# Performance work log

Hardware: AMD Instinct MI355X
Metric: run time of the kernel (lower is better)

## Reference

```python
import jax, jax.numpy as jnp
import numpy as np

HEADS = 16
HEAD_DIM = 64
DIM = 1024
INNER = HEADS * HEAD_DIM  # 1024


def rotate_half(t):
    # split last dim into two halves, return cat(-x2, x1)
    x1, x2 = jnp.split(t, 2, axis=-1)
    return jnp.concatenate((-x2, x1), axis=-1)


def rope_table(n, head_dim, dtype):
    inv_freq = 1.0 / (10000.0 ** (jnp.arange(0, head_dim, 2, dtype=jnp.float32) / head_dim))
    freqs = jnp.arange(n, dtype=jnp.float32)[:, None] * inv_freq[None, :]  # [n, hd/2]
    return jnp.concatenate((freqs, freqs), axis=-1).astype(dtype)  # [n, hd]


def setup_inputs() -> dict:
    key = jax.random.key(0)
    k1, k2, k3, k4 = jax.random.split(key, 4)
    x = jax.random.normal(k1, (1, 4096, DIM), dtype=jnp.float32)
    s = 0.02
    W_qkv = jax.random.normal(k2, (DIM, 3 * INNER), dtype=jnp.float32) * s
    W_o1 = jax.random.normal(k3, (INNER, DIM), dtype=jnp.float32) * s
    W_o2 = jax.random.normal(k4, (DIM, DIM), dtype=jnp.float32) * s
    gamma = jnp.ones((DIM,), dtype=jnp.float32)
    return {"x": x, "W_qkv": W_qkv, "W_o1": W_o1, "W_o2": W_o2, "gamma": gamma}


def reference(x, W_qkv, W_o1, W_o2, gamma):
    b, n, _ = x.shape
    scale = HEAD_DIM ** -0.5
    qkv = x @ W_qkv  # [b, n, 3*inner]
    q, k, v = jnp.split(qkv, 3, axis=-1)
    # [b, n, inner] -> [b, h, n, hd]
    to_heads = lambda t: t.reshape(b, n, HEADS, HEAD_DIM).transpose(0, 2, 1, 3)
    q, k, v = to_heads(q), to_heads(k), to_heads(v)

    pos = rope_table(n, HEAD_DIM, x.dtype)  # [n, hd]
    cos, sin = jnp.cos(pos), jnp.sin(pos)
    apply_rope = lambda t: t * cos + rotate_half(t) * sin
    q, k = apply_rope(q), apply_rope(k)

    dots = jnp.einsum('bhid,bhjd->bhij', q, k) * scale  # [b, h, n, n]
    causal = jnp.triu(jnp.ones((n, n), dtype=bool), 1)
    neg = -jnp.finfo(dots.dtype).max
    dots = jnp.where(causal, neg, dots)
    attn = jax.nn.softmax(dots, axis=-1)

    out = jnp.einsum('bhij,bhjd->bhid', attn, v)  # [b, h, n, hd]
    out = out.transpose(0, 2, 1, 3).reshape(b, n, INNER)
    # to_out: Linear -> ReLU -> Linear (dropout = identity in eval)
    out = jax.nn.relu(out @ W_o1) @ W_o2
    # AttnLayerNorm: layer_norm over last dim with gamma, beta=0
    mean = jnp.mean(out, axis=-1, keepdims=True)
    var = jnp.var(out, axis=-1, keepdims=True)
    out = (out - mean) * jax.lax.rsqrt(var + 1e-5) * gamma
    return out
```

## Files before the change

### kernel.cpp

```cpp
#include <hip/hip_runtime.h>
#include <hip/hip_bf16.h>
#include <float.h>
#include <math.h>

#define HEADS 16
#define HD 64
#define DIM 1024
#define NTOK 4096
#define QKVN 3072

typedef short s8v __attribute__((ext_vector_type(8)));
typedef float f4v __attribute__((ext_vector_type(4)));

static __device__ __forceinline__ unsigned short f2b(float f) {
  __hip_bfloat16 h = __float2bfloat16(f);
  unsigned short u;
  __builtin_memcpy(&u, &h, 2);
  return u;
}
static __device__ __forceinline__ s8v pack_bf8(float4 a, float4 b) {
  s8v r;
  r[0] = (short)f2b(a.x); r[1] = (short)f2b(a.y); r[2] = (short)f2b(a.z); r[3] = (short)f2b(a.w);
  r[4] = (short)f2b(b.x); r[5] = (short)f2b(b.y); r[6] = (short)f2b(b.z); r[7] = (short)f2b(b.w);
  return r;
}
static __device__ __forceinline__ void gload16(const unsigned short* g, unsigned short* l) {
  __builtin_amdgcn_global_load_lds(
      (const __attribute__((address_space(1))) void*)g,
      (__attribute__((address_space(3))) void*)l, 16, 0, 0);
}

__global__ __launch_bounds__(256) void cast_f2b(const float* __restrict__ in,
                                                unsigned short* __restrict__ out) {
  const int i = (blockIdx.x * 256 + threadIdx.x) * 8;
  float4 a = *(const float4*)(in + i);
  float4 b = *(const float4*)(in + i + 4);
  *(s8v*)(out + i) = pack_bf8(a, b);
}

__global__ __launch_bounds__(256) void transpose_f2b(const float* __restrict__ in,
                                                     unsigned short* __restrict__ out,
                                                     int K, int N) {
  __shared__ unsigned short T[32][36];
  const int k0 = blockIdx.y * 32, n0 = blockIdx.x * 32;
  const int t = threadIdx.x;
  const int r = t >> 3, c4 = (t & 7) * 4;
  float4 f = *(const float4*)(in + (size_t)(k0 + r) * N + n0 + c4);
  T[r][c4 + 0] = f2b(f.x);
  T[r][c4 + 1] = f2b(f.y);
  T[r][c4 + 2] = f2b(f.z);
  T[r][c4 + 3] = f2b(f.w);
  __syncthreads();
  ushort4 o;
  o.x = T[c4 + 0][r];
  o.y = T[c4 + 1][r];
  o.z = T[c4 + 2][r];
  o.w = T[c4 + 3][r];
  *(ushort4*)(out + (size_t)(n0 + r) * K + k0 + c4) = o;
}

template <int OUT_F32, int RELU>
__global__ __launch_bounds__(256) void gemm_bb(const unsigned short* __restrict__ A,
                                               const unsigned short* __restrict__ Bt,
                                               void* __restrict__ Cv,
                                               int M, int N, int K) {
  __shared__ __align__(16) unsigned short As[128 * 32];
  __shared__ __align__(16) unsigned short Bs[128 * 32];
  const int t = threadIdx.x;
  const int wave = t >> 6, lane = t & 63;
  const int wr = wave >> 1, wc = wave & 1;
  const int g = lane >> 4, c = lane & 15;
  const int m0 = blockIdx.y * 128, n0 = blockIdx.x * 128;

  const int sr = t >> 2;
  const int sc = (t & 3) * 8;

  const unsigned short* a0p = A + (size_t)(m0 + sr) * K + sc;
  const unsigned short* a1p = A + (size_t)(m0 + sr + 64) * K + sc;
  const unsigned short* b0p = Bt + (size_t)(n0 + sr) * K + sc;
  const unsigned short* b1p = Bt + (size_t)(n0 + sr + 64) * K + sc;
  unsigned short* lA0 = As + t * 8;
  unsigned short* lA1 = As + 2048 + t * 8;
  unsigned short* lB0 = Bs + t * 8;
  unsigned short* lB1 = Bs + 2048 + t * 8;

  f4v acc[4][4] = {};

  for (int k0 = 0; k0 < K; k0 += 32) {
    __syncthreads();
    gload16(a0p + k0, lA0);
    gload16(a1p + k0, lA1);
    gload16(b0p + k0, lB0);
    gload16(b1p + k0, lB1);
    __syncthreads();
    s8v af[4], bf[4];
#pragma unroll
    for (int m = 0; m < 4; ++m) af[m] = *(const s8v*)&As[(wr * 64 + m * 16 + c) * 32 + g * 8];
#pragma unroll
    for (int n = 0; n < 4; ++n) bf[n] = *(const s8v*)&Bs[(wc * 64 + n * 16 + c) * 32 + g * 8];
#pragma unroll
    for (int m = 0; m < 4; ++m)
#pragma unroll
      for (int n = 0; n < 4; ++n)
        acc[m][n] = __builtin_amdgcn_mfma_f32_16x16x32_bf16(af[m], bf[n], acc[m][n], 0, 0, 0);
  }

#pragma unroll
  for (int m = 0; m < 4; ++m)
#pragma unroll
    for (int n = 0; n < 4; ++n)
#pragma unroll
      for (int r = 0; r < 4; ++r) {
        const int row = m0 + wr * 64 + m * 16 + g * 4 + r;
        const int col = n0 + wc * 64 + n * 16 + c;
        float v = acc[m][n][r];
        if (RELU) v = fmaxf(v, 0.f);
        if (OUT_F32)
          ((float*)Cv)[(size_t)row * N + col] = v;
        else
          ((unsigned short*)Cv)[(size_t)row * N + col] = f2b(v);
      }
}

__global__ __launch_bounds__(512) void rope64_kernel(unsigned short* __restrict__ qkv) {
  __shared__ float cs[32], sn[32];
  const int i = blockIdx.x;
  const int t = threadIdx.x;
  if (t < 32) {
    const double inv = pow(10000.0, -(double)t / 32.0);
    double sd, cd;
    sincos((double)i * inv, &sd, &cd);
    cs[t] = (float)cd;
    sn[t] = (float)sd;
  }
  __syncthreads();
  const int h = t >> 5, j = t & 31;
  const float cc = cs[j], ss = sn[j];
  const size_t base = (size_t)i * QKVN + h * HD + j;
  const float qa = __bfloat162float(*(const __hip_bfloat16*)&qkv[base]);
  const float qb = __bfloat162float(*(const __hip_bfloat16*)&qkv[base + 32]);
  qkv[base] = f2b((qa * cc - qb * ss) * 0.125f);
  qkv[base + 32] = f2b((qb * cc + qa * ss) * 0.125f);
  const float ka = __bfloat162float(*(const __hip_bfloat16*)&qkv[base + DIM]);
  const float kb = __bfloat162float(*(const __hip_bfloat16*)&qkv[base + DIM + 32]);
  qkv[base + DIM] = f2b(ka * cc - kb * ss);
  qkv[base + DIM + 32] = f2b(kb * cc + ka * ss);
}

__global__ __launch_bounds__(256) void attn_mfma(const unsigned short* __restrict__ qkv,
                                                 unsigned short* __restrict__ att) {
  __shared__ unsigned short Ks[64][72];
  __shared__ unsigned short Vt[64][72];
  __shared__ unsigned short Pl[4][16][72];
  const int bid = blockIdx.x;
  const int h = bid & 15;
  const int qi = 63 - (bid >> 4);
  const int t = threadIdx.x;
  const int w = t >> 6, lane = t & 63;
  const int g = lane >> 4, c = lane & 15;
  const int q0 = qi * 64 + w * 16;

  s8v qf[2];
#pragma unroll
  for (int kf = 0; kf < 2; ++kf)
    qf[kf] = *(const s8v*)(qkv + (size_t)(q0 + c) * QKVN + h * HD + kf * 32 + g * 8);

  f4v O[4] = {};
  float mrow[4], lrow[4];
#pragma unroll
  for (int r = 0; r < 4; ++r) { mrow[r] = -1e30f; lrow[r] = 0.f; }

  const int ntile = qi + 1;
  for (int tile = 0; tile < ntile; ++tile) {
    const int kv0 = tile * 64;
    __syncthreads();
    {
      const int kr = t >> 3;
      const int kc = (t & 7) * 8;
#pragma unroll
      for (int it = 0; it < 2; ++it) {
        const int r = kr + it * 32;
        *(s8v*)&Ks[r][kc] =
            *(const s8v*)(qkv + (size_t)(kv0 + r) * QKVN + DIM + h * HD + kc);
      }
      const int kg = t & 15, dc = t >> 4;
      const unsigned short* vb = qkv + (size_t)(kv0 + 4 * kg) * QKVN + 2 * DIM + h * HD + dc * 4;
      ushort4 v0 = *(const ushort4*)(vb);
      ushort4 v1 = *(const ushort4*)(vb + QKVN);
      ushort4 v2 = *(const ushort4*)(vb + 2 * QKVN);
      ushort4 v3 = *(const ushort4*)(vb + 3 * QKVN);
      const unsigned short* r0 = (const unsigned short*)&v0;
      const unsigned short* r1 = (const unsigned short*)&v1;
      const unsigned short* r2 = (const unsigned short*)&v2;
      const unsigned short* r3 = (const unsigned short*)&v3;
#pragma unroll
      for (int dl = 0; dl < 4; ++dl) {
        ushort4 u;
        u.x = r0[dl]; u.y = r1[dl]; u.z = r2[dl]; u.w = r3[dl];
        *(ushort4*)&Vt[dc * 4 + dl][kg * 4] = u;
      }
    }
    __syncthreads();

    f4v S[4] = {};
#pragma unroll
    for (int n = 0; n < 4; ++n)
#pragma unroll
      for (int kf = 0; kf < 2; ++kf) {
        s8v kfr = *(const s8v*)&Ks[n * 16 + c][kf * 32 + g * 8];
        S[n] = __builtin_amdgcn_mfma_f32_16x16x32_bf16(qf[kf], kfr, S[n], 0, 0, 0);
      }

    float rmax[4] = {-1e30f, -1e30f, -1e30f, -1e30f};
    if (kv0 + 63 > q0) {
#pragma unroll
      for (int n = 0; n < 4; ++n)
#pragma unroll
        for (int r = 0; r < 4; ++r) {
          float s = S[n][r];
          const int col = kv0 + n * 16 + c;
          const int row = q0 + 4 * g + r;
          s = (col > row) ? -1e30f : s;
          S[n][r] = s;
          rmax[r] = fmaxf(rmax[r], s);
        }
    } else {
#pragma unroll
      for (int n = 0; n < 4; ++n)
#pragma unroll
        for (int r = 0; r < 4; ++r) rmax[r] = fmaxf(rmax[r], S[n][r]);
    }
#pragma unroll
    for (int r = 0; r < 4; ++r) {
      rmax[r] = fmaxf(rmax[r], __shfl_xor(rmax[r], 1));
      rmax[r] = fmaxf(rmax[r], __shfl_xor(rmax[r], 2));
      rmax[r] = fmaxf(rmax[r], __shfl_xor(rmax[r], 4));
      rmax[r] = fmaxf(rmax[r], __shfl_xor(rmax[r], 8));
    }

    bool upd = false;
#pragma unroll
    for (int r = 0; r < 4; ++r) upd = upd || (rmax[r] > mrow[r] + 8.0f);
    if (__any((int)upd)) {
#pragma unroll
      for (int r = 0; r < 4; ++r) {
        const float mn = fmaxf(mrow[r], rmax[r]);
        const float corr = __expf(mrow[r] - mn);
        mrow[r] = mn;
        lrow[r] *= corr;
#pragma unroll
        for (int n = 0; n < 4; ++n) O[n][r] *= corr;
      }
    }
    float rsum[4] = {0.f, 0.f, 0.f, 0.f};
#pragma unroll
    for (int n = 0; n < 4; ++n)
#pragma unroll
      for (int r = 0; r < 4; ++r) {
        const float p = __expf(S[n][r] - mrow[r]);
        rsum[r] += p;
        Pl[w][4 * g + r][n * 16 + c] = f2b(p);
      }
#pragma unroll
    for (int r = 0; r < 4; ++r) {
      rsum[r] += __shfl_xor(rsum[r], 1);
      rsum[r] += __shfl_xor(rsum[r], 2);
      rsum[r] += __shfl_xor(rsum[r], 4);
      rsum[r] += __shfl_xor(rsum[r], 8);
      lrow[r] += rsum[r];
    }

    s8v pf[2];
#pragma unroll
    for (int kf = 0; kf < 2; ++kf) pf[kf] = *(const s8v*)&Pl[w][c][kf * 32 + g * 8];
#pragma unroll
    for (int n = 0; n < 4; ++n)
#pragma unroll
      for (int kf = 0; kf < 2; ++kf) {
        s8v vf = *(const s8v*)&Vt[n * 16 + c][kf * 32 + g * 8];
        O[n] = __builtin_amdgcn_mfma_f32_16x16x32_bf16(pf[kf], vf, O[n], 0, 0, 0);
      }
  }

  float inv[4];
#pragma unroll
  for (int r = 0; r < 4; ++r) inv[r] = 1.f / lrow[r];
#pragma unroll
  for (int n = 0; n < 4; ++n)
#pragma unroll
    for (int r = 0; r < 4; ++r) {
      const int row = q0 + 4 * g + r;
      att[(size_t)row * DIM + h * HD + n * 16 + c] = f2b(O[n][r] * inv[r]);
    }
}

__global__ __launch_bounds__(256) void layernorm_kernel(const float* __restrict__ x,
                                                        const float* __restrict__ gamma,
                                                        float* __restrict__ out) {
  const int row = blockIdx.x;
  const int t = threadIdx.x;
  const float4 v = ((const float4*)(x + (size_t)row * DIM))[t];
  float s = v.x + v.y + v.z + v.w;
  float ss = v.x * v.x + v.y * v.y + v.z * v.z + v.w * v.w;
#pragma unroll
  for (int off = 32; off > 0; off >>= 1) {
    s += __shfl_xor(s, off);
    ss += __shfl_xor(ss, off);
  }
  __shared__ float red[8];
  const int wave = t >> 6, lane = t & 63;
  if (lane == 0) {
    red[wave] = s;
    red[4 + wave] = ss;
  }
  __syncthreads();
  const float S = red[0] + red[1] + red[2] + red[3];
  const float SS = red[4] + red[5] + red[6] + red[7];
  const float mean = S * (1.f / 1024.f);
  const float var = SS * (1.f / 1024.f) - mean * mean;
  const float r = rsqrtf(var + 1e-5f);
  const float4 g4 = ((const float4*)gamma)[t];
  float4 o;
  o.x = (v.x - mean) * r * g4.x;
  o.y = (v.y - mean) * r * g4.y;
  o.z = (v.z - mean) * r * g4.z;
  o.w = (v.w - mean) * r * g4.w;
  ((float4*)(out + (size_t)row * DIM))[t] = o;
}

extern "C" void kernel_launch(void* const* d_in, const int* in_sizes, int n_in,
                              void* d_out, int out_size, void* d_ws, size_t ws_size,
                              hipStream_t stream) {
  const float* x = (const float*)d_in[0];
  const float* Wqkv = (const float*)d_in[1];
  const float* Wo1 = (const float*)d_in[2];
  const float* Wo2 = (const float*)d_in[3];
  const float* gamma = (const float*)d_in[4];
  float* out = (float*)d_out;

  char* wsb = (char*)d_ws;
  unsigned short* xb = (unsigned short*)wsb;
  unsigned short* qkv = (unsigned short*)(wsb + 8388608ull);
  unsigned short* Wqkvt = (unsigned short*)(wsb + 33554432ull);
  unsigned short* Wo1t = (unsigned short*)(wsb + 39845888ull);
  unsigned short* Wo2t = (unsigned short*)(wsb + 41943040ull);
  unsigned short* att = (unsigned short*)wsb;
  unsigned short* h1 = (unsigned short*)(wsb + 8388608ull);
  float* h2 = (float*)(wsb + 16777216ull);

  cast_f2b<<<NTOK * DIM / (256 * 8), 256, 0, stream>>>(x, xb);
  transpose_f2b<<<dim3(QKVN / 32, DIM / 32), 256, 0, stream>>>(Wqkv, Wqkvt, DIM, QKVN);
  transpose_f2b<<<dim3(DIM / 32, DIM / 32), 256, 0, stream>>>(Wo1, Wo1t, DIM, DIM);
  transpose_f2b<<<dim3(DIM / 32, DIM / 32), 256, 0, stream>>>(Wo2, Wo2t, DIM, DIM);
  gemm_bb<0, 0><<<dim3(QKVN / 128, NTOK / 128), 256, 0, stream>>>(xb, Wqkvt, qkv, NTOK, QKVN, DIM);
  rope64_kernel<<<NTOK, 512, 0, stream>>>(qkv);
  attn_mfma<<<NTOK / 64 * HEADS, 256, 0, stream>>>(qkv, att);
  gemm_bb<0, 1><<<dim3(DIM / 128, NTOK / 128), 256, 0, stream>>>(att, Wo1t, h1, NTOK, DIM, DIM);
  gemm_bb<1, 0><<<dim3(DIM / 128, NTOK / 128), 256, 0, stream>>>(h1, Wo2t, h2, NTOK, DIM, DIM);
  layernorm_kernel<<<NTOK, 256, 0, stream>>>(h2, gamma, out);
}
```

Before: 343.6 us.

## Process 128 query rows per attention block and prefetch next K/V tile into registers

The attention kernel now gives each block 128 query rows, with each wave owning two 16-row strips, so every K/V tile staged in shared memory is reused by twice as many queries. It also prefetches the next K/V tile into registers while the current tile is being computed, overlapping global loads with MFMA work. Strips that lie fully above the causal diagonal skip their compute. The trade-offs are half as many blocks (1024 → 512), higher register pressure, and coarser causal load imbalance across blocks.

Result: slower. 418.4 us (+21.8%).

```diff
diff --git a/kernel.cpp b/kernel.cpp
--- a/kernel.cpp
+++ b/kernel.cpp
@@ -151,147 +151,197 @@
                                                  unsigned short* __restrict__ att) {
   __shared__ unsigned short Ks[64][72];
   __shared__ unsigned short Vt[64][72];
-  __shared__ unsigned short Pl[4][16][72];
+  __shared__ unsigned short Pl[4][32][72];
   const int bid = blockIdx.x;
   const int h = bid & 15;
-  const int qi = 63 - (bid >> 4);
+  const int qi = 31 - (bid >> 4);
   const int t = threadIdx.x;
   const int w = t >> 6, lane = t & 63;
   const int g = lane >> 4, c = lane & 15;
-  const int q0 = qi * 64 + w * 16;
-
-  s8v qf[2];
-#pragma unroll
-  for (int kf = 0; kf < 2; ++kf)
-    qf[kf] = *(const s8v*)(qkv + (size_t)(q0 + c) * QKVN + h * HD + kf * 32 + g * 8);
-
-  f4v O[4] = {};
-  float mrow[4], lrow[4];
-#pragma unroll
-  for (int r = 0; r < 4; ++r) { mrow[r] = -1e30f; lrow[r] = 0.f; }
-
-  const int ntile = qi + 1;
+  const int q0 = qi * 128;
+  const int base0 = q0 + w * 16;
+  const int base1 = q0 + 64 + w * 16;
+  const int base_m[2] = {base0, base1};
+
+  s8v qf[2][2];
+#pragma unroll
+  for (int m = 0; m < 2; ++m)
+#pragma unroll
+    for (int kf = 0; kf < 2; ++kf)
+      qf[m][kf] = *(const s8v*)(qkv + (size_t)(base_m[m] + c) * QKVN + h * HD + kf * 32 + g * 8);
+
+  f4v O[2][4] = {};
+  float mrow[2][4], lrow[2][4];
+#pragma unroll
+  for (int m = 0; m < 2; ++m)
+#pragma unroll
+    for (int r = 0; r < 4; ++r) { mrow[m][r] = -1e30f; lrow[m][r] = 0.f; }
+
+  const int ntile = 2 * qi + 2;
+
+  const int kr = t >> 3, kc = (t & 7) * 8;
+  const int kg = t & 15, dc = t >> 4;
+  s8v kreg0, kreg1;
+  ushort4 vr0, vr1, vr2, vr3;
+  {
+    const unsigned short* kbp = qkv + (size_t)kr * QKVN + DIM + h * HD + kc;
+    kreg0 = *(const s8v*)(kbp);
+    kreg1 = *(const s8v*)(kbp + 32 * QKVN);
+    const unsigned short* vb = qkv + (size_t)(4 * kg) * QKVN + 2 * DIM + h * HD + dc * 4;
+    vr0 = *(const ushort4*)(vb);
+    vr1 = *(const ushort4*)(vb + QKVN);
+    vr2 = *(const ushort4*)(vb + 2 * QKVN);
+    vr3 = *(const ushort4*)(vb + 3 * QKVN);
+  }
+
   for (int tile = 0; tile < ntile; ++tile) {
     const int kv0 = tile * 64;
     __syncthreads();
+    *(s8v*)&Ks[kr][kc] = kreg0;
+    *(s8v*)&Ks[kr + 32][kc] = kreg1;
     {
-      const int kr = t >> 3;
-      const int kc = (t & 7) * 8;
-#pragma unroll
-      for (int it = 0; it < 2; ++it) {
-        const int r = kr + it * 32;
-        *(s8v*)&Ks[r][kc] =
-            *(const s8v*)(qkv + (size_t)(kv0 + r) * QKVN + DIM + h * HD + kc);
-      }
-      const int kg = t & 15, dc = t >> 4;
-      const unsigned short* vb = qkv + (size_t)(kv0 + 4 * kg) * QKVN + 2 * DIM + h * HD + dc * 4;
-      ushort4 v0 = *(const ushort4*)(vb);
-      ushort4 v1 = *(const ushort4*)(vb + QKVN);
-      ushort4 v2 = *(const ushort4*)(vb + 2 * QKVN);
-      ushort4 v3 = *(const ushort4*)(vb + 3 * QKVN);
-      const unsigned short* r0 = (const unsigned short*)&v0;
-      const unsigned short* r1 = (const unsigned short*)&v1;
-      const unsigned short* r2 = (const unsigned short*)&v2;
-      const unsigned short* r3 = (const unsigned short*)&v3;
+      const unsigned short* q0v = (const unsigned short*)&vr0;
+      const unsigned short* q1v = (const unsigned short*)&vr1;
+      const unsigned short* q2v = (const unsigned short*)&vr2;
+      const unsigned short* q3v = (const unsigned short*)&vr3;
 #pragma unroll
       for (int dl = 0; dl < 4; ++dl) {
         ushort4 u;
-        u.x = r0[dl]; u.y = r1[dl]; u.z = r2[dl]; u.w = r3[dl];
+        u.x = q0v[dl]; u.y = q1v[dl]; u.z = q2v[dl]; u.w = q3v[dl];
         *(ushort4*)&Vt[dc * 4 + dl][kg * 4] = u;
       }
     }
     __syncthreads();
-
-    f4v S[4] = {};
+    if (tile + 1 < ntile) {
+      const int nv0 = kv0 + 64;
+      const unsigned short* kbp = qkv + (size_t)(nv0 + kr) * QKVN + DIM + h * HD + kc;
+      kreg0 = *(const s8v*)(kbp);
+      kreg1 = *(const s8v*)(kbp + 32 * QKVN);
+      const unsigned short* vb = qkv + (size_t)(nv0 + 4 * kg) * QKVN + 2 * DIM + h * HD + dc * 4;
+      vr0 = *(const ushort4*)(vb);
+      vr1 = *(const ushort4*)(vb + QKVN);
+      vr2 = *(const ushort4*)(vb + 2 * QKVN);
+      vr3 = *(const ushort4*)(vb + 3 * QKVN);
+    }
+
+    f4v S[2][4];
+    float rmax[2][4];
+    bool act[2];
+#pragma unroll
+    for (int m = 0; m < 2; ++m) {
+      act[m] = (kv0 <= base_m[m] + 15);
+#pragma unroll
+      for (int r = 0; r < 4; ++r) rmax[m][r] = -1e30f;
+    }
+#pragma unroll
+    for (int m = 0; m < 2; ++m) {
+      if (!act[m]) continue;
+#pragma unroll
+      for (int n = 0; n < 4; ++n) {
+        S[m][n] = f4v{0.f, 0.f, 0.f, 0.f};
+#pragma unroll
+        for (int kf = 0; kf < 2; ++kf) {
+          s8v kfr = *(const s8v*)&Ks[n * 16 + c][kf * 32 + g * 8];
+          S[m][n] = __builtin_amdgcn_mfma_f32_16x16x32_bf16(qf[m][kf], kfr, S[m][n], 0, 0, 0);
+        }
+      }
+      if (kv0 + 63 > base_m[m]) {
+#pragma unroll
+        for (int n = 0; n < 4; ++n)
+#pragma unroll
+          for (int r = 0; r < 4; ++r) {
+            float s = S[m][n][r];
+            const int col = kv0 + n * 16 + c;
+            const int row = base_m[m] + 4 * g + r;
+            s = (col > row) ? -1e30f : s;
+            S[m][n][r] = s;
+            rmax[m][r] = fmaxf(rmax[m][r], s);
+          }
+      } else {
+#pragma unroll
+        for (int n = 0; n < 4; ++n)
+#pragma unroll
+          for (int r = 0; r < 4; ++r) rmax[m][r] = fmaxf(rmax[m][r], S[m][n][r]);
+      }
+#pragma unroll
+      for (int r = 0; r < 4; ++r) {
+        rmax[m][r] = fmaxf(rmax[m][r], __shfl_xor(rmax[m][r], 1));
+        rmax[m][r] = fmaxf(rmax[m][r], __shfl_xor(rmax[m][r], 2));
+        rmax[m][r] = fmaxf(rmax[m][r], __shfl_xor(rmax[m][r], 4));
+        rmax[m][r] = fmaxf(rmax[m][r], __shfl_xor(rmax[m][r], 8));
+      }
+    }
+
+    bool upd = false;
+#pragma unroll
+    for (int m = 0; m < 2; ++m)
+#pragma unroll
+      for (int r = 0; r < 4; ++r) upd = upd || (rmax[m][r] > mrow[m][r] + 8.0f);
+    if (__any((int)upd)) {
+#pragma unroll
+      for (int m = 0; m < 2; ++m)
+#pragma unroll
+        for (int r = 0; r < 4; ++r) {
+          const float mn = fmaxf(mrow[m][r], rmax[m][r]);
+          const float corr = __expf(mrow[m][r] - mn);
+          mrow[m][r] = mn;
+          lrow[m][r] *= corr;
+#pragma unroll
+          for (int n = 0; n < 4; ++n) O[m][n][r] *= corr;
+        }
+    }
+
+#pragma unroll
+    for (int m = 0; m < 2; ++m) {
+      if (!act[m]) continue;
+      float rsum[4] = {0.f, 0.f, 0.f, 0.f};
+#pragma unroll
+      for (int n = 0; n < 4; ++n)
+#pragma unroll
+        for (int r = 0; r < 4; ++r) {
+          const float p = __expf(S[m][n][r] - mrow[m][r]);
+          rsum[r] += p;
+          Pl[w][m * 16 + 4 * g + r][n * 16 + c] = f2b(p);
+        }
+#pragma unroll
+      for (int r = 0; r < 4; ++r) {
+        rsum[r] += __shfl_xor(rsum[r], 1);
+        rsum[r] += __shfl_xor(rsum[r], 2);
+        rsum[r] += __shfl_xor(rsum[r], 4);
+        rsum[r] += __shfl_xor(rsum[r], 8);
+        lrow[m][r] += rsum[r];
+      }
+    }
+
+#pragma unroll
+    for (int m = 0; m < 2; ++m) {
+      if (!act[m]) continue;
+      s8v pf[2];
+#pragma unroll
+      for (int kf = 0; kf < 2; ++kf) pf[kf] = *(const s8v*)&Pl[w][m * 16 + c][kf * 32 + g * 8];
+#pragma unroll
+      for (int n = 0; n < 4; ++n)
+#pragma unroll
+        for (int kf = 0; kf < 2; ++kf) {
+          s8v vf = *(const s8v*)&Vt[n * 16 + c][kf * 32 + g * 8];
+          O[m][n] = __builtin_amdgcn_mfma_f32_16x16x32_bf16(pf[kf], vf, O[m][n], 0, 0, 0);
+        }
+    }
+  }
+
+#pragma unroll
+  for (int m = 0; m < 2; ++m) {
+    float inv[4];
+#pragma unroll
+    for (int r = 0; r < 4; ++r) inv[r] = 1.f / lrow[m][r];
 #pragma unroll
     for (int n = 0; n < 4; ++n)
 #pragma unroll
-      for (int kf = 0; kf < 2; ++kf) {
-        s8v kfr = *(const s8v*)&Ks[n * 16 + c][kf * 32 + g * 8];
-        S[n] = __builtin_amdgcn_mfma_f32_16x16x32_bf16(qf[kf], kfr, S[n], 0, 0, 0);
-      }
-
-    float rmax[4] = {-1e30f, -1e30f, -1e30f, -1e30f};
-    if (kv0 + 63 > q0) {
-#pragma unroll
-      for (int n = 0; n < 4; ++n)
-#pragma unroll
-        for (int r = 0; r < 4; ++r) {
-          float s = S[n][r];
-          const int col = kv0 + n * 16 + c;
-          const int row = q0 + 4 * g + r;
-          s = (col > row) ? -1e30f : s;
-          S[n][r] = s;
-          rmax[r] = fmaxf(rmax[r], s);
-        }
-    } else {
-#pragma unroll
-      for (int n = 0; n < 4; ++n)
-#pragma unroll
-        for (int r = 0; r < 4; ++r) rmax[r] = fmaxf(rmax[r], S[n][r]);
-    }
-#pragma unroll
-    for (int r = 0; r < 4; ++r) {
-      rmax[r] = fmaxf(rmax[r], __shfl_xor(rmax[r], 1));
-      rmax[r] = fmaxf(rmax[r], __shfl_xor(rmax[r], 2));
-      rmax[r] = fmaxf(rmax[r], __shfl_xor(rmax[r], 4));
-      rmax[r] = fmaxf(rmax[r], __shfl_xor(rmax[r], 8));
-    }
-
-    bool upd = false;
-#pragma unroll
-    for (int r = 0; r < 4; ++r) upd = upd || (rmax[r] > mrow[r] + 8.0f);
-    if (__any((int)upd)) {
-#pragma unroll
       for (int r = 0; r < 4; ++r) {
-        const float mn = fmaxf(mrow[r], rmax[r]);
-        const float corr = __expf(mrow[r] - mn);
-        mrow[r] = mn;
-        lrow[r] *= corr;
-#pragma unroll
-        for (int n = 0; n < 4; ++n) O[n][r] *= corr;
-      }
-    }
-    float rsum[4] = {0.f, 0.f, 0.f, 0.f};
-#pragma unroll
-    for (int n = 0; n < 4; ++n)
-#pragma unroll
-      for (int r = 0; r < 4; ++r) {
-        const float p = __expf(S[n][r] - mrow[r]);
-        rsum[r] += p;
-        Pl[w][4 * g + r][n * 16 + c] = f2b(p);
-      }
-#pragma unroll
-    for (int r = 0; r < 4; ++r) {
-      rsum[r] += __shfl_xor(rsum[r], 1);
-      rsum[r] += __shfl_xor(rsum[r], 2);
-      rsum[r] += __shfl_xor(rsum[r], 4);
-      rsum[r] += __shfl_xor(rsum[r], 8);
-      lrow[r] += rsum[r];
-    }
-
-    s8v pf[2];
-#pragma unroll
-    for (int kf = 0; kf < 2; ++kf) pf[kf] = *(const s8v*)&Pl[w][c][kf * 32 + g * 8];
-#pragma unroll
-    for (int n = 0; n < 4; ++n)
-#pragma unroll
-      for (int kf = 0; kf < 2; ++kf) {
-        s8v vf = *(const s8v*)&Vt[n * 16 + c][kf * 32 + g * 8];
-        O[n] = __builtin_amdgcn_mfma_f32_16x16x32_bf16(pf[kf], vf, O[n], 0, 0, 0);
-      }
-  }
-
-  float inv[4];
-#pragma unroll
-  for (int r = 0; r < 4; ++r) inv[r] = 1.f / lrow[r];
-#pragma unroll
-  for (int n = 0; n < 4; ++n)
-#pragma unroll
-    for (int r = 0; r < 4; ++r) {
-      const int row = q0 + 4 * g + r;
-      att[(size_t)row * DIM + h * HD + n * 16 + c] = f2b(O[n][r] * inv[r]);
-    }
+        const int row = base_m[m] + 4 * g + r;
+        att[(size_t)row * DIM + h * HD + n * 16 + c] = f2b(O[m][n][r] * inv[r]);
+      }
+  }
 }
 
 __global__ __launch_bounds__(256) void layernorm_kernel(const float* __restrict__ x,
@@ -354,7 +404,7 @@
   transpose_f2b<<<dim3(DIM / 32, DIM / 32), 256, 0, stream>>>(Wo2, Wo2t, DIM, DIM);
   gemm_bb<0, 0><<<dim3(QKVN / 128, NTOK / 128), 256, 0, stream>>>(xb, Wqkvt, qkv, NTOK, QKVN, DIM);
   rope64_kernel<<<NTOK, 512, 0, stream>>>(qkv);
-  attn_mfma<<<NTOK / 64 * HEADS, 256, 0, stream>>>(qkv, att);
+  attn_mfma<<<NTOK / 128 * HEADS, 256, 0, stream>>>(qkv, att);
   gemm_bb<0, 1><<<dim3(DIM / 128, NTOK / 128), 256, 0, stream>>>(att, Wo1t, h1, NTOK, DIM, DIM);
   gemm_bb<1, 0><<<dim3(DIM / 128, NTOK / 128), 256, 0, stream>>>(h1, Wo2t, h2, NTOK, DIM, DIM);
   layernorm_kernel<<<NTOK, 256, 0, stream>>>(h2, gamma, out);
```
